# Performance work log

Measured on AMD Instinct MI355X. Metric: run time of the kernel, lower is better.

Reference implementation:

```python
import jax, jax.numpy as jnp
import numpy as np
from itertools import product

MAX_ALLOC = [3, 3, 3, 3, 3, 3]   # env.maximum_allocation -> 4^6 = 4096 actions
NUM_SESSIONS = 64
STATE_DIM = NUM_SESSIONS + len(MAX_ALLOC)  # 70
HIDDEN = (1024, 1024)
BATCH = 8192


def setup_inputs() -> dict:
    key = jax.random.key(0)
    ks = jax.random.split(key, 8)
    # states: sessions part uniform [0,1); waitlist part uniform [0,4) so mask is nontrivial
    sessions = jax.random.uniform(ks[0], (BATCH, NUM_SESSIONS), dtype=jnp.float32)
    waitlist = jax.random.uniform(ks[1], (BATCH, len(MAX_ALLOC)), dtype=jnp.float32) * 4.0
    states = jnp.concatenate([sessions, waitlist], axis=1)
    # enumerated action space, same order as itertools.product in the torch module
    action_space = jnp.asarray(
        np.array(list(product(*[range(m + 1) for m in MAX_ALLOC])), dtype=np.int32))  # [4096, 6]
    A = action_space.shape[0]
    W1 = jax.random.normal(ks[2], (STATE_DIM, HIDDEN[0]), dtype=jnp.float32) / np.sqrt(STATE_DIM)
    b1 = jnp.zeros((HIDDEN[0],), dtype=jnp.float32)
    W2 = jax.random.normal(ks[3], (HIDDEN[0], HIDDEN[1]), dtype=jnp.float32) / np.sqrt(HIDDEN[0])
    b2 = jnp.zeros((HIDDEN[1],), dtype=jnp.float32)
    Wh = jax.random.normal(ks[4], (HIDDEN[1], A), dtype=jnp.float32) / np.sqrt(HIDDEN[1])
    bh = jnp.zeros((A,), dtype=jnp.float32)
    return {"states": states, "W1": W1, "b1": b1, "W2": W2, "b2": b2,
            "Wh": Wh, "bh": bh, "action_space": action_space,
            "num_sessions": NUM_SESSIONS}


def reference(states, W1, b1, W2, b2, Wh, bh, action_space, num_sessions):
    # vectorized get_action_mask: action j is feasible for row i iff all(action_j <= waitlist_i)
    waitlist = states[:, num_sessions:]                                   # [B, 6]
    feasible = jnp.all(action_space[None, :, :].astype(states.dtype)
                       <= waitlist[:, None, :], axis=-1)                  # [B, A] bool
    mask = feasible.astype(states.dtype)
    # tanh MLP
    h = jnp.tanh(states @ W1 + b1)
    h = jnp.tanh(h @ W2 + b2)
    logits = h @ Wh + bh + jnp.log(mask + 1e-9)                           # [B, A]
    return jax.nn.softmax(logits, axis=1)
```

## Files before the change

### kernel.cpp

```cpp
#include <hip/hip_runtime.h>
#include <hip/hip_bf16.h>
#include <math.h>

using bf16 = __hip_bfloat16;
typedef __attribute__((ext_vector_type(8))) short short8;
typedef __attribute__((ext_vector_type(4))) float f32x4;
typedef __attribute__((ext_vector_type(4))) unsigned int u32x4;

#define BATCH 8192
#define SDIM  70
#define NS    64
#define NW    6
#define HID   1024
#define NA    4096
#define KPAD  96

__device__ __forceinline__ void gld_lds16(const bf16* g, bf16* l) {
    __builtin_amdgcn_global_load_lds(
        (const __attribute__((address_space(1))) void*)g,
        (__attribute__((address_space(3))) void*)l, 16, 0, 0);
}


__global__ __launch_bounds__(256)
void cvt_states_k(const float* __restrict__ s, bf16* __restrict__ o) {
    int idx = blockIdx.x * 256 + threadIdx.x;
    int row = idx / KPAD;
    int col = idx - row * KPAD;
    float v = (col < SDIM) ? s[row * SDIM + col] : 0.0f;
    o[idx] = __float2bfloat16(v);
}

__global__ __launch_bounds__(256)
void transpose_cvt_k(const float* __restrict__ in, bf16* __restrict__ out,
                     int K, int N, int Kpad) {
    __shared__ float tile[32][33];
    int kb = blockIdx.y * 32, nb = blockIdx.x * 32;
    int tx = threadIdx.x, ty = threadIdx.y;
    #pragma unroll
    for (int i = 0; i < 32; i += 8) {
        int k = kb + ty + i, n = nb + tx;
        tile[ty + i][tx] = (k < K) ? in[(size_t)k * N + n] : 0.0f;
    }
    __syncthreads();
    #pragma unroll
    for (int i = 0; i < 32; i += 8) {
        int n = nb + ty + i, k = kb + tx;
        if (k < Kpad) out[(size_t)n * Kpad + k] = __float2bfloat16(tile[tx][ty + i]);
    }
}

__global__ __launch_bounds__(256)
void pack_act_k(const int* __restrict__ act, unsigned* __restrict__ pact) {
    int c = blockIdx.x * 256 + threadIdx.x;
    if (c < NA) {
        const int* a = act + c * 6;
        unsigned p = 0;
        #pragma unroll
        for (int i = 0; i < 6; i++) p |= ((unsigned)a[i]) << (5 * i);
        pact[c] = p;
    }
}

template<int MODE>
__global__ __launch_bounds__(256)
void gemm128(const bf16* __restrict__ A, const bf16* __restrict__ BT,
             const float* __restrict__ bias, void* __restrict__ Cout,
             int M, int N, int K) {
    const int n0 = blockIdx.x * 128;
    const int m0 = blockIdx.y * 128;
    const int tid  = threadIdx.x;
    const int wave = tid >> 6;
    const int lane = tid & 63;

    __shared__ __align__(16) bf16 As[128 * 32];
    __shared__ __align__(16) bf16 Bs[128 * 32];

    const int srow = wave * 32 + (lane >> 2);
    const int sk   = (lane & 3) * 8;
    const bf16* ag = A  + (size_t)(m0 + srow) * K + sk;
    const bf16* bg = BT + (size_t)(n0 + srow) * K + sk;
    bf16* asl = &As[(wave * 32) * 32];
    bf16* bsl = &Bs[(wave * 32) * 32];

    f32x4 acc[4][4];
    #pragma unroll
    for (int i = 0; i < 4; i++)
        #pragma unroll
        for (int j = 0; j < 4; j++) acc[i][j] = (f32x4){0.f, 0.f, 0.f, 0.f};

    const int rb = (wave >> 1) * 64;
    const int cb = (wave & 1) * 64;
    const int fr = lane & 15;
    const int koff = (lane >> 4) * 8;

    for (int k0 = 0; k0 < K; k0 += 32) {
        gld_lds16(ag + k0,          asl);
        gld_lds16(ag + k0 + 16 * K, asl + 16 * 32);
        gld_lds16(bg + k0,          bsl);
        gld_lds16(bg + k0 + 16 * K, bsl + 16 * 32);
        __syncthreads();

        short8 af[4], bf[4];
        #pragma unroll
        for (int i = 0; i < 4; i++)
            af[i] = *(const short8*)&As[(rb + i * 16 + fr) * 32 + koff];
        #pragma unroll
        for (int j = 0; j < 4; j++)
            bf[j] = *(const short8*)&Bs[(cb + j * 16 + fr) * 32 + koff];
        #pragma unroll
        for (int i = 0; i < 4; i++)
            #pragma unroll
            for (int j = 0; j < 4; j++)
                acc[i][j] = __builtin_amdgcn_mfma_f32_16x16x32_bf16(af[i], bf[j], acc[i][j], 0, 0, 0);
        __syncthreads();
    }

    const int orow = m0 + rb + (lane >> 4) * 4;
    const int ocol = n0 + cb + fr;
    #pragma unroll
    for (int j = 0; j < 4; j++) {
        int col = ocol + j * 16;
        float bv = bias[col];
        #pragma unroll
        for (int i = 0; i < 4; i++) {
            int rbase = orow + i * 16;
            #pragma unroll
            for (int r = 0; r < 4; r++) {
                float val = acc[i][j][r] + bv;
                size_t off = (size_t)(rbase + r) * N + col;
                if (MODE == 0)      ((bf16*)Cout)[off] = __float2bfloat16(tanhf(val));
                else if (MODE == 1) ((float*)Cout)[off] = val;
                else                ((bf16*)Cout)[off] = __float2bfloat16(val);
            }
        }
    }
}

__global__ __launch_bounds__(256)
void masked_softmax_k(const bf16* __restrict__ logitsb, float* __restrict__ out,
                      const float* __restrict__ states,
                      const unsigned* __restrict__ pact) {
    const int row  = blockIdx.x;
    const int t    = threadIdx.x;
    const int lane = t & 63, wave = t >> 6;

    __shared__ float redm[4], reds[4];
    __shared__ float smax, ssum;

    const float* wl = states + (size_t)row * SDIM + NS;
    unsigned T = 0;
    #pragma unroll
    for (int i = 0; i < 6; i++) T |= ((unsigned)(int)wl[i]) << (5 * i);
    const unsigned H  = 0x21084210u;
    const unsigned TH = T | H;

    const unsigned* lrow = (const unsigned*)(logitsb + (size_t)row * NA) + t * 8;
    u32x4 raw0 = *(const u32x4*)lrow;
    u32x4 raw1 = *(const u32x4*)(lrow + 4);
    unsigned rw[8];
    #pragma unroll
    for (int i = 0; i < 4; i++) { rw[i] = raw0[i]; rw[4 + i] = raw1[i]; }

    float v[16];
    #pragma unroll
    for (int i = 0; i < 8; i++) {
        v[2 * i]     = __uint_as_float(rw[i] << 16);
        v[2 * i + 1] = __uint_as_float(rw[i] & 0xffff0000u);
    }

    const unsigned* prow = pact + t * 16;
    float lmax = -1e30f;
    #pragma unroll
    for (int q = 0; q < 4; q++) {
        u32x4 p = *(const u32x4*)(prow + q * 4);
        #pragma unroll
        for (int e = 0; e < 4; e++) {
            int j = q * 4 + e;
            bool f = (((TH - p[e]) & H) == H);
            float lg = v[j] + (f ? 0.0f : -20.7232658f);
            v[j] = lg;
            lmax = fmaxf(lmax, lg);
        }
    }
    #pragma unroll
    for (int o = 32; o > 0; o >>= 1) lmax = fmaxf(lmax, __shfl_down(lmax, o, 64));
    if (lane == 0) redm[wave] = lmax;
    __syncthreads();
    if (t == 0) smax = fmaxf(fmaxf(redm[0], redm[1]), fmaxf(redm[2], redm[3]));
    __syncthreads();
    const float bmax = smax;

    float s = 0.f;
    #pragma unroll
    for (int j = 0; j < 16; j++) { float ev = __expf(v[j] - bmax); v[j] = ev; s += ev; }
    #pragma unroll
    for (int o = 32; o > 0; o >>= 1) s += __shfl_down(s, o, 64);
    if (lane == 0) reds[wave] = s;
    __syncthreads();
    if (t == 0) ssum = reds[0] + reds[1] + reds[2] + reds[3];
    __syncthreads();
    const float inv = 1.0f / ssum;

    float* orow = out + (size_t)row * NA + t * 16;
    #pragma unroll
    for (int q = 0; q < 4; q++) {
        f32x4 o4 = { v[q * 4] * inv, v[q * 4 + 1] * inv,
                     v[q * 4 + 2] * inv, v[q * 4 + 3] * inv };
        *(f32x4*)(orow + q * 4) = o4;
    }
}

extern "C" void kernel_launch(void* const* d_in, const int* in_sizes, int n_in,
                              void* d_out, int out_size, void* d_ws, size_t ws_size,
                              hipStream_t stream) {
    const float* states = (const float*)d_in[0];
    const float* W1 = (const float*)d_in[1];
    const float* b1 = (const float*)d_in[2];
    const float* W2 = (const float*)d_in[3];
    const float* b2 = (const float*)d_in[4];
    const float* Wh = (const float*)d_in[5];
    const float* bh = (const float*)d_in[6];
    const int*   act = (const int*)d_in[7];
    float* out = (float*)d_out;

    char* ws = (char*)d_ws;
    bf16* statesb = (bf16*)ws; ws += (size_t)BATCH * KPAD * 2;
    bf16* w1bt    = (bf16*)ws; ws += (size_t)HID * KPAD * 2;
    bf16* w2bt    = (bf16*)ws; ws += (size_t)HID * HID * 2;
    bf16* whbt    = (bf16*)ws; ws += (size_t)NA * HID * 2;
    bf16* h1      = (bf16*)ws; ws += (size_t)BATCH * HID * 2;
    bf16* h2      = (bf16*)ws; ws += (size_t)BATCH * HID * 2;
    bf16* logitsb = (bf16*)ws; ws += (size_t)BATCH * NA * 2;
    unsigned* pact = (unsigned*)ws; ws += (size_t)NA * 4;

    dim3 tb(32, 8);
    cvt_states_k<<<(BATCH * KPAD) / 256, 256, 0, stream>>>(states, statesb);
    transpose_cvt_k<<<dim3(HID / 32, KPAD / 32), tb, 0, stream>>>(W1, w1bt, SDIM, HID, KPAD);
    transpose_cvt_k<<<dim3(HID / 32, HID / 32), tb, 0, stream>>>(W2, w2bt, HID, HID, HID);
    transpose_cvt_k<<<dim3(NA / 32, HID / 32), tb, 0, stream>>>(Wh, whbt, HID, NA, HID);
    pack_act_k<<<NA / 256, 256, 0, stream>>>(act, pact);

    gemm128<0><<<dim3(HID / 128, BATCH / 128), 256, 0, stream>>>(statesb, w1bt, b1, h1, BATCH, HID, KPAD);
    gemm128<0><<<dim3(HID / 128, BATCH / 128), 256, 0, stream>>>(h1, w2bt, b2, h2, BATCH, HID, HID);
    gemm128<2><<<dim3(NA / 128, BATCH / 128), 256, 0, stream>>>(h2, whbt, bh, logitsb, BATCH, NA, HID);

    masked_softmax_k<<<BATCH, 256, 0, stream>>>(logitsb, out, states, pact);
}
```

Baseline: 353.5 us.

## Widen GEMM K-tile to 64 with XOR-swizzled LDS and fuse prep kernels

The GEMM now stages a 64-wide K slice per iteration instead of 32, which halves the number of barrier pairs. It uses an XOR swizzle on the LDS chunk index to avoid bank conflicts on the fragment reads. The five prep kernels (state conversion, three weight transposes, action packing) are merged into one launch dispatched by block index, which cuts launch overhead. KPAD is raised to 128 so the first layer's K is a multiple of 64, at the cost of extra zero-padding work and double the LDS per block.

```diff
diff --git a/kernel.cpp b/kernel.cpp
--- a/kernel.cpp
+++ b/kernel.cpp
@@ -10,10 +10,9 @@
 #define BATCH 8192
 #define SDIM  70
 #define NS    64
-#define NW    6
 #define HID   1024
 #define NA    4096
-#define KPAD  96
+#define KPAD  128
 
 __device__ __forceinline__ void gld_lds16(const bf16* g, bf16* l) {
     __builtin_amdgcn_global_load_lds(
@@ -21,22 +20,11 @@
         (__attribute__((address_space(3))) void*)l, 16, 0, 0);
 }
 
-
-__global__ __launch_bounds__(256)
-void cvt_states_k(const float* __restrict__ s, bf16* __restrict__ o) {
-    int idx = blockIdx.x * 256 + threadIdx.x;
-    int row = idx / KPAD;
-    int col = idx - row * KPAD;
-    float v = (col < SDIM) ? s[row * SDIM + col] : 0.0f;
-    o[idx] = __float2bfloat16(v);
-}
-
-__global__ __launch_bounds__(256)
-void transpose_cvt_k(const float* __restrict__ in, bf16* __restrict__ out,
-                     int K, int N, int Kpad) {
-    __shared__ float tile[32][33];
-    int kb = blockIdx.y * 32, nb = blockIdx.x * 32;
-    int tx = threadIdx.x, ty = threadIdx.y;
+__device__ __forceinline__ void tr32(const float* __restrict__ in, bf16* __restrict__ out,
+                                     int K, int N, int Kpad, int bx, int by, int t,
+                                     float (*tile)[33]) {
+    int kb = by * 32, nb = bx * 32;
+    int tx = t & 31, ty = t >> 5;
     #pragma unroll
     for (int i = 0; i < 32; i += 8) {
         int k = kb + ty + i, n = nb + tx;
@@ -51,14 +39,37 @@
 }
 
 __global__ __launch_bounds__(256)
-void pack_act_k(const int* __restrict__ act, unsigned* __restrict__ pact) {
-    int c = blockIdx.x * 256 + threadIdx.x;
-    if (c < NA) {
-        const int* a = act + c * 6;
-        unsigned p = 0;
-        #pragma unroll
-        for (int i = 0; i < 6; i++) p |= ((unsigned)a[i]) << (5 * i);
-        pact[c] = p;
+void prep_k(const float* __restrict__ states, const float* __restrict__ W1,
+            const float* __restrict__ W2, const float* __restrict__ Wh,
+            const int* __restrict__ act,
+            bf16* __restrict__ statesb, bf16* __restrict__ w1bt,
+            bf16* __restrict__ w2bt, bf16* __restrict__ whbt,
+            unsigned* __restrict__ pact) {
+    __shared__ float tile[32][33];
+    const int b = blockIdx.x, t = threadIdx.x;
+    if (b < 4096) {
+        int idx = b * 256 + t;
+        int row = idx >> 7, col = idx & 127;
+        float v = (col < SDIM) ? states[row * SDIM + col] : 0.0f;
+        statesb[idx] = __float2bfloat16(v);
+    } else if (b < 4224) {
+        int r = b - 4096;
+        tr32(W1, w1bt, SDIM, HID, KPAD, r & 31, r >> 5, t, tile);
+    } else if (b < 5248) {
+        int r = b - 4224;
+        tr32(W2, w2bt, HID, HID, HID, r & 31, r >> 5, t, tile);
+    } else if (b < 9344) {
+        int r = b - 5248;
+        tr32(Wh, whbt, HID, NA, HID, r & 127, r >> 7, t, tile);
+    } else {
+        int c = (b - 9344) * 256 + t;
+        if (c < NA) {
+            const int* a = act + c * 6;
+            unsigned p = 0;
+            #pragma unroll
+            for (int i = 0; i < 6; i++) p |= ((unsigned)a[i]) << (5 * i);
+            pact[c] = p;
+        }
     }
 }
 
@@ -73,15 +84,13 @@
     const int wave = tid >> 6;
     const int lane = tid & 63;
 
-    __shared__ __align__(16) bf16 As[128 * 32];
-    __shared__ __align__(16) bf16 Bs[128 * 32];
-
-    const int srow = wave * 32 + (lane >> 2);
-    const int sk   = (lane & 3) * 8;
-    const bf16* ag = A  + (size_t)(m0 + srow) * K + sk;
-    const bf16* bg = BT + (size_t)(n0 + srow) * K + sk;
-    bf16* asl = &As[(wave * 32) * 32];
-    bf16* bsl = &Bs[(wave * 32) * 32];
+    __shared__ __align__(16) bf16 As[128 * 64];
+    __shared__ __align__(16) bf16 Bs[128 * 64];
+
+    const int lr = lane >> 3;
+    const int gk = ((lane & 7) ^ lr) * 8;
+    const bf16* ag = A  + (size_t)(m0 + lr) * K + gk;
+    const bf16* bg = BT + (size_t)(n0 + lr) * K + gk;
 
     f32x4 acc[4][4];
     #pragma unroll
@@ -92,27 +101,37 @@
     const int rb = (wave >> 1) * 64;
     const int cb = (wave & 1) * 64;
     const int fr = lane & 15;
-    const int koff = (lane >> 4) * 8;
-
-    for (int k0 = 0; k0 < K; k0 += 32) {
-        gld_lds16(ag + k0,          asl);
-        gld_lds16(ag + k0 + 16 * K, asl + 16 * 32);
-        gld_lds16(bg + k0,          bsl);
-        gld_lds16(bg + k0 + 16 * K, bsl + 16 * 32);
+    const int kq = lane >> 4;
+
+    for (int k0 = 0; k0 < K; k0 += 64) {
+        #pragma unroll
+        for (int q = 0; q < 4; q++) {
+            const int ch = q * 4 + wave;
+            gld_lds16(ag + (size_t)(ch * 8) * K + k0, &As[ch * 512]);
+            gld_lds16(bg + (size_t)(ch * 8) * K + k0, &Bs[ch * 512]);
+        }
         __syncthreads();
 
-        short8 af[4], bf[4];
-        #pragma unroll
-        for (int i = 0; i < 4; i++)
-            af[i] = *(const short8*)&As[(rb + i * 16 + fr) * 32 + koff];
-        #pragma unroll
-        for (int j = 0; j < 4; j++)
-            bf[j] = *(const short8*)&Bs[(cb + j * 16 + fr) * 32 + koff];
-        #pragma unroll
-        for (int i = 0; i < 4; i++)
-            #pragma unroll
-            for (int j = 0; j < 4; j++)
-                acc[i][j] = __builtin_amdgcn_mfma_f32_16x16x32_bf16(af[i], bf[j], acc[i][j], 0, 0, 0);
+        #pragma unroll
+        for (int kk = 0; kk < 2; kk++) {
+            const int cbase = kk * 4 + kq;
+            short8 af[4], bfr[4];
+            #pragma unroll
+            for (int i = 0; i < 4; i++) {
+                int r = rb + i * 16 + fr;
+                af[i] = *(const short8*)&As[r * 64 + ((cbase ^ (r & 7)) * 8)];
+            }
+            #pragma unroll
+            for (int j = 0; j < 4; j++) {
+                int r = cb + j * 16 + fr;
+                bfr[j] = *(const short8*)&Bs[r * 64 + ((cbase ^ (r & 7)) * 8)];
+            }
+            #pragma unroll
+            for (int i = 0; i < 4; i++)
+                #pragma unroll
+                for (int j = 0; j < 4; j++)
+                    acc[i][j] = __builtin_amdgcn_mfma_f32_16x16x32_bf16(af[i], bfr[j], acc[i][j], 0, 0, 0);
+        }
         __syncthreads();
     }
 
@@ -234,12 +253,8 @@
     bf16* logitsb = (bf16*)ws; ws += (size_t)BATCH * NA * 2;
     unsigned* pact = (unsigned*)ws; ws += (size_t)NA * 4;
 
-    dim3 tb(32, 8);
-    cvt_states_k<<<(BATCH * KPAD) / 256, 256, 0, stream>>>(states, statesb);
-    transpose_cvt_k<<<dim3(HID / 32, KPAD / 32), tb, 0, stream>>>(W1, w1bt, SDIM, HID, KPAD);
-    transpose_cvt_k<<<dim3(HID / 32, HID / 32), tb, 0, stream>>>(W2, w2bt, HID, HID, HID);
-    transpose_cvt_k<<<dim3(NA / 32, HID / 32), tb, 0, stream>>>(Wh, whbt, HID, NA, HID);
-    pack_act_k<<<NA / 256, 256, 0, stream>>>(act, pact);
+    prep_k<<<9360, 256, 0, stream>>>(states, W1, W2, Wh, act,
+                                     statesb, w1bt, w2bt, whbt, pact);
 
     gemm128<0><<<dim3(HID / 128, BATCH / 128), 256, 0, stream>>>(statesb, w1bt, b1, h1, BATCH, HID, KPAD);
     gemm128<0><<<dim3(HID / 128, BATCH / 128), 256, 0, stream>>>(h1, w2bt, b2, h2, BATCH, HID, HID);
```

Result: faster. 337.6 us (-4.5%).
